# Kernel optimization log

Measured on AMD Instinct MI355X. Metric: run time of the kernel, lower is better.

The kernel has to match this reference:

```python
import jax, jax.numpy as jnp
import numpy as np

NUM_GROUPS = 8
EPS = 1e-5


def group_norm(x, gamma, beta):
    # x: [B, C, H, W]
    B, C, H, W = x.shape
    xg = x.reshape(B, NUM_GROUPS, C // NUM_GROUPS, H, W)
    mean = xg.mean(axis=(2, 3, 4), keepdims=True)
    var = xg.var(axis=(2, 3, 4), keepdims=True)
    xn = (xg - mean) * jax.lax.rsqrt(var + EPS)
    xn = xn.reshape(B, C, H, W)
    return xn * gamma[None, :, None, None] + beta[None, :, None, None]


def setup_inputs() -> dict:
    key = jax.random.key(0)
    ks = jax.random.split(key, 7)
    B, C, H, W = 4, 512, 64, 64
    x = jax.random.normal(ks[0], (B, C, H, W), dtype=jnp.float32)
    gamma = jnp.ones((C,), dtype=jnp.float32)
    beta = jnp.zeros((C,), dtype=jnp.float32)
    w_qkv = jax.random.normal(ks[1], (3 * C, C), dtype=jnp.float32) * (1.0 / np.sqrt(C))
    b_qkv = jax.random.normal(ks[2], (3 * C,), dtype=jnp.float32) * 0.01
    w_proj = jax.random.normal(ks[3], (C, C), dtype=jnp.float32) * (1.0 / np.sqrt(C))
    b_proj = jax.random.normal(ks[4], (C,), dtype=jnp.float32) * 0.01
    return {"x": x, "gamma": gamma, "beta": beta, "w_qkv": w_qkv,
            "b_qkv": b_qkv, "w_proj": w_proj, "b_proj": b_proj}


def reference(x, gamma, beta, w_qkv, b_qkv, w_proj, b_proj):
    B, C, H, W = x.shape
    N = H * W
    h = group_norm(x, gamma, beta)                       # [B,C,H,W]
    hf = h.reshape(B, C, N)                              # [B,C,N]
    # 1x1 conv == channel-wise linear map
    qkv = jnp.einsum('oc,bcn->bon', w_qkv, hf) + b_qkv[None, :, None]  # [B,3C,N]
    q, k, v = jnp.split(qkv, 3, axis=1)                  # each [B,C,N]
    q = q.transpose(0, 2, 1)                             # [B,N,C]
    v = v.transpose(0, 2, 1)                             # [B,N,C]
    scale = C ** (-0.5)
    attn = jax.nn.softmax(jnp.einsum('bnc,bcm->bnm', q, k) * scale, axis=-1)  # [B,N,N]
    out = jnp.einsum('bnm,bmc->bnc', attn, v)            # [B,N,C]
    out = out.transpose(0, 2, 1).reshape(B, C, H, W)
    proj = jnp.einsum('oc,bchw->bohw', w_proj, out) + b_proj[None, :, None, None]
    return x + proj
```

## Files before the change

### kernel.cpp

```cpp
#include <hip/hip_runtime.h>

typedef __attribute__((ext_vector_type(8))) short bf16x8;
typedef __attribute__((ext_vector_type(4))) float f32x4;
typedef __attribute__((ext_vector_type(4))) short s16x4;
using u16 = unsigned short;
using u8 = unsigned char;

#define DEVINL static __device__ __forceinline__

DEVINL u16 f2bf(float f) {
  union { float f; unsigned u; } v; v.f = f;
  unsigned r = v.u + 0x7FFFu + ((v.u >> 16) & 1u);
  return (u16)(r >> 16);
}

DEVINL u8 f2e4m3_sw(float f) {
  union { float f; unsigned u; } v; v.f = f;
  unsigned s = (v.u >> 24) & 0x80u;
  float a = fabsf(f);
  a = fminf(a, 448.f);
  union { float f; unsigned u; } b; b.f = a;
  unsigned bu = b.u + 0x7FFFFu + ((b.u >> 20) & 1u);
  unsigned e = bu >> 23;
  unsigned r;
  if (e >= 121) {
    r = ((e - 120) << 3) | ((bu >> 20) & 7u);
    if (r > 0x7Eu) r = 0x7Eu;
  } else {
    r = (unsigned)(a * 512.f + 0.5f);
    if (r > 7u) r = 8u;
  }
  return (u8)(r | s);
}

#if __has_builtin(__builtin_amdgcn_cvt_pk_fp8_f32)
DEVINL u8 f2e4m3(float f) {
  int p = __builtin_amdgcn_cvt_pk_fp8_f32(f, f, 0, false);
  return (u8)(p & 0xFF);
}
#else
DEVINL u8 f2e4m3(float f) { return f2e4m3_sw(f); }
#endif

DEVINL float bf2f(u16 h) {
  union { unsigned u; float f; } v; v.u = ((unsigned)h) << 16; return v.f;
}

DEVINL void gload16(const u16* g, u16* l) {
  __builtin_amdgcn_global_load_lds((const __attribute__((address_space(1))) void*)g,
                                   (__attribute__((address_space(3))) void*)l,
                                   16, 0, 0);
}
DEVINL void gload16b(const u8* g, u8* l) {
  __builtin_amdgcn_global_load_lds((const __attribute__((address_space(1))) void*)g,
                                   (__attribute__((address_space(3))) void*)l,
                                   16, 0, 0);
}

__global__ __launch_bounds__(256) void gn_stats1_k(const float* __restrict__ x,
                                                   float* __restrict__ psum,
                                                   float* __restrict__ psumsq) {
  const int blk = blockIdx.x;
  const float4* p4 = (const float4*)(x + (size_t)(blk >> 4) * (64 * 4096))
                     + (size_t)(blk & 15) * 4096;
  float s = 0.f, ss = 0.f;
  #pragma unroll
  for (int i = 0; i < 16; ++i) {
    float4 v = p4[i*256 + threadIdx.x];
    s  += v.x + v.y + v.z + v.w;
    ss += v.x*v.x + v.y*v.y + v.z*v.z + v.w*v.w;
  }
  #pragma unroll
  for (int off = 32; off > 0; off >>= 1) {
    s  += __shfl_down(s, off, 64);
    ss += __shfl_down(ss, off, 64);
  }
  __shared__ float rs[4], rss[4];
  const int lane = threadIdx.x & 63, w = threadIdx.x >> 6;
  if (lane == 0) { rs[w] = s; rss[w] = ss; }
  __syncthreads();
  if (threadIdx.x == 0) {
    psum[blk]   = rs[0]+rs[1]+rs[2]+rs[3];
    psumsq[blk] = rss[0]+rss[1]+rss[2]+rss[3];
  }
}

__global__ void gn_stats2_k(const float* __restrict__ psum,
                            const float* __restrict__ psumsq,
                            float* __restrict__ stats) {
  const int bg = threadIdx.x;
  if (bg >= 32) return;
  float s = 0.f, ss = 0.f;
  #pragma unroll
  for (int p = 0; p < 16; ++p) { s += psum[bg*16+p]; ss += psumsq[bg*16+p]; }
  const float inv = 1.f / 262144.f;
  float mean = s * inv;
  float var  = ss * inv - mean * mean;
  stats[bg*2]   = mean;
  stats[bg*2+1] = rsqrtf(var + 1e-5f);
}

__global__ __launch_bounds__(256) void gn_apply_k(const float* __restrict__ x,
                                                  const float* __restrict__ gamma,
                                                  const float* __restrict__ beta,
                                                  const float* __restrict__ stats,
                                                  u16* __restrict__ hT,
                                                  u8* __restrict__ hT8, int useF8) {
  __shared__ u16 tile[64][68];
  const int b = blockIdx.z, ct = blockIdx.y, nt = blockIdx.x;
  const int t = threadIdx.x;
  const float mean = stats[(b*8 + ct)*2 + 0];
  const float rstd = stats[(b*8 + ct)*2 + 1];
  const float* xb = x + ((size_t)b*512 + (size_t)ct*64) * 4096 + nt*64;
  #pragma unroll
  for (int i = 0; i < 4; ++i) {
    int idx = i*256 + t;
    int cl = idx >> 4, nl4 = idx & 15;
    float4 v = *(const float4*)(xb + (size_t)cl*4096 + nl4*4);
    float g = gamma[ct*64 + cl], bb = beta[ct*64 + cl];
    s16x4 o;
    o.x = (short)f2bf((v.x - mean) * rstd * g + bb);
    o.y = (short)f2bf((v.y - mean) * rstd * g + bb);
    o.z = (short)f2bf((v.z - mean) * rstd * g + bb);
    o.w = (short)f2bf((v.w - mean) * rstd * g + bb);
    *(s16x4*)(&tile[cl][nl4*4]) = o;
  }
  __syncthreads();
  if (useF8) {
    u8* o = hT8 + ((size_t)b*4096 + (size_t)nt*64) * 512 + ct*64;
    #pragma unroll
    for (int i = 0; i < 16; ++i) {
      int idx = i*256 + t; int nl = idx >> 6, cl = idx & 63;
      o[(size_t)nl*512 + cl] = f2e4m3(bf2f(tile[cl][nl]));
    }
  } else {
    u16* o = hT + ((size_t)b*4096 + (size_t)nt*64) * 512 + ct*64;
    #pragma unroll
    for (int i = 0; i < 16; ++i) {
      int idx = i*256 + t; int nl = idx >> 6, cl = idx & 63;
      o[(size_t)nl*512 + cl] = tile[cl][nl];
    }
  }
}

__global__ __launch_bounds__(256) void cast_w_k(const float* __restrict__ wq,
                                                const float* __restrict__ wp,
                                                u16* __restrict__ wqb,
                                                u16* __restrict__ wpb,
                                                u8* __restrict__ wq8,
                                                u8* __restrict__ wp8, int useF8) {
  int i = blockIdx.x*256 + threadIdx.x;
  if (useF8) {
    if (i < 1536*512) wq8[i] = f2e4m3(wq[i]);
    if (i < 512*512)  wp8[i] = f2e4m3(wp[i]);
  } else {
    if (i < 1536*512) wqb[i] = f2bf(wq[i]);
    if (i < 512*512)  wpb[i] = f2bf(wp[i]);
  }
}

DEVINL void gemm_nt_core(const u16* __restrict__ A, int lda,
                         const u16* __restrict__ B, int ldb,
                         int K, u16* As, u16* Bs, f32x4 acc[4][4]) {
  const int tid = threadIdx.x;
  const int lane = tid & 63, w = tid >> 6;
  const int wr = w >> 1, wc = w & 1;
  const int fr = lane & 15, fk = lane >> 4;
  for (int kt = 0; kt < K; kt += 64) {
    #pragma unroll
    for (int i = 0; i < 4; ++i) {
      int ch = i*256 + tid;
      int row = ch >> 3, kc = ch & 7;
      gload16(A + (size_t)row*lda + kt + kc*8, As + ch*8);
      gload16(B + (size_t)row*ldb + kt + kc*8, Bs + ch*8);
    }
    __syncthreads();
    #pragma unroll
    for (int kk = 0; kk < 2; ++kk) {
      bf16x8 af[4], bfg[4];
      #pragma unroll
      for (int i = 0; i < 4; ++i)
        af[i] = *(const bf16x8*)(As + ((wr*64 + i*16 + fr)*64 + kk*32 + fk*8));
      #pragma unroll
      for (int j = 0; j < 4; ++j)
        bfg[j] = *(const bf16x8*)(Bs + ((wc*64 + j*16 + fr)*64 + kk*32 + fk*8));
      #pragma unroll
      for (int i = 0; i < 4; ++i)
        #pragma unroll
        for (int j = 0; j < 4; ++j)
          acc[i][j] = __builtin_amdgcn_mfma_f32_16x16x32_bf16(af[i], bfg[j], acc[i][j], 0, 0, 0);
    }
    __syncthreads();
  }
}

#define GEMM_PROLOGUE() \
  __shared__ __align__(16) u16 As[128*64]; \
  __shared__ __align__(16) u16 Bs[128*64]; \
  f32x4 acc[4][4] = {}; \
  const int tid = threadIdx.x; \
  const int lane = tid & 63, w = tid >> 6; \
  const int wr = w >> 1, wc = w & 1; \
  const int fr = lane & 15, fk = lane >> 4; \
  (void)lane;

#define MFMA8(a, b, c) __builtin_amdgcn_mfma_f32_16x16x32_fp8_fp8((a), (b), (c), 0, 0, 0)

DEVINL void gemm_nt_f8(const u8* __restrict__ A, int lda,
                       const u8* __restrict__ B, int ldb,
                       int K, u8* Af, u8* Bf, f32x4 acc[4][4]) {
  const int tid = threadIdx.x;
  const int lane = tid & 63, w = tid >> 6;
  const int wr = w >> 1, wc = w & 1;
  const int fr = lane & 15, fk = lane >> 4;
  for (int kt = 0; kt < K; kt += 128) {
    #pragma unroll
    for (int q = 0; q < 4; ++q) {
      int c = q*256 + tid;
      int row = c >> 3, s16 = c & 7;
      int kc = s16 ^ ((row >> 1) & 7);
      gload16b(A + (size_t)row*lda + kt + kc*16, Af + c*16);
      gload16b(B + (size_t)row*ldb + kt + kc*16, Bf + c*16);
    }
    __syncthreads();
    #pragma unroll
    for (int kk = 0; kk < 4; ++kk) {
      long long a8[4], b8[4];
      #pragma unroll
      for (int i = 0; i < 4; ++i) {
        int row = wr*64 + i*16 + fr;
        int s16r = (kk*2 + (fk>>1)) ^ ((row>>1)&7);
        a8[i] = *(const long long*)(Af + row*128 + (s16r<<4) + ((fk&1)<<3));
      }
      #pragma unroll
      for (int j = 0; j < 4; ++j) {
        int row = wc*64 + j*16 + fr;
        int s16r = (kk*2 + (fk>>1)) ^ ((row>>1)&7);
        b8[j] = *(const long long*)(Bf + row*128 + (s16r<<4) + ((fk&1)<<3));
      }
      #pragma unroll
      for (int i = 0; i < 4; ++i)
        #pragma unroll
        for (int j = 0; j < 4; ++j)
          acc[i][j] = MFMA8(a8[i], b8[j], acc[i][j]);
    }
    __syncthreads();
  }
}

__global__ __launch_bounds__(256) void k_qkv(const u16* __restrict__ hT,
                                             const u16* __restrict__ wq,
                                             const float* __restrict__ bqkv,
                                             u16* __restrict__ qT, u16* __restrict__ kT,
                                             u16* __restrict__ vb) {
  GEMM_PROLOGUE();
  const int bz = blockIdx.z;
  const int rowBase = blockIdx.y * 128, colBase = blockIdx.x * 128;
  gemm_nt_core(hT + ((size_t)bz*4096 + rowBase)*512, 512,
               wq + (size_t)colBase*512, 512, 512, As, Bs, acc);
  #pragma unroll
  for (int i = 0; i < 4; ++i)
    #pragma unroll
    for (int j = 0; j < 4; ++j)
      #pragma unroll
      for (int r = 0; r < 4; ++r) {
        int n = rowBase + wr*64 + i*16 + fk*4 + r;
        int o = colBase + wc*64 + j*16 + fr;
        u16 u = f2bf(acc[i][j][r] + bqkv[o]);
        if (o < 512)       qT[((size_t)bz*4096 + n)*512 + o]          = u;
        else if (o < 1024) kT[((size_t)bz*4096 + n)*512 + (o - 512)]  = u;
        else               vb[((size_t)bz*512 + (o - 1024))*4096 + n] = u;
      }
}

__global__ __launch_bounds__(256) void k_qkv_f8(const u8* __restrict__ hT8,
                                                const u8* __restrict__ wq8,
                                                const float* __restrict__ bqkv,
                                                u8* __restrict__ qF8, u8* __restrict__ kF8,
                                                u8* __restrict__ vF8) {
  __shared__ __align__(16) u8 Af[128*128];
  __shared__ __align__(16) u8 Bf[128*128];
  f32x4 acc[4][4] = {};
  const int tid = threadIdx.x;
  const int lane = tid & 63, w = tid >> 6;
  const int wr = w >> 1, wc = w & 1;
  const int fr = lane & 15, fk = lane >> 4;
  const int bz = blockIdx.z;
  const int rowBase = blockIdx.y * 128, colBase = blockIdx.x * 128;
  gemm_nt_f8(hT8 + ((size_t)bz*4096 + rowBase)*512, 512,
             wq8 + (size_t)colBase*512, 512, 512, Af, Bf, acc);
  #pragma unroll
  for (int i = 0; i < 4; ++i)
    #pragma unroll
    for (int j = 0; j < 4; ++j)
      #pragma unroll
      for (int r = 0; r < 4; ++r) {
        int n = rowBase + wr*64 + i*16 + fk*4 + r;
        int o = colBase + wc*64 + j*16 + fr;
        u8 u = f2e4m3(acc[i][j][r] + bqkv[o]);
        if (o < 512)       qF8[((size_t)bz*4096 + n)*512 + o]          = u;
        else if (o < 1024) kF8[((size_t)bz*4096 + n)*512 + (o - 512)]  = u;
        else               vF8[((size_t)bz*512 + (o - 1024))*4096 + n] = u;
      }
}

__global__ __launch_bounds__(512) void k_scores_f8(const u8* __restrict__ qF8,
                                                   const u8* __restrict__ kF8,
                                                   u8* __restrict__ E8,
                                                   float* __restrict__ lsum) {
  __shared__ __align__(16) u8 Af[128*64];
  __shared__ __align__(16) u8 Bf[128*64];
  f32x4 acc[2][4] = {};
  const int tid = threadIdx.x;
  const int lane = tid & 63, w = tid >> 6;
  const int wr = w >> 1, wc = w & 1;
  const int fr = lane & 15, fk = lane >> 4;
  const int bz = blockIdx.z;
  int f = blockIdx.y * 32 + blockIdx.x;
  int L = (f & 7) * 128 + (f >> 3);
  const int rowBase = (L >> 5) * 128, colBase = (L & 31) * 128;
  const u8* qa = qF8 + (size_t)bz*4096*512 + (size_t)rowBase*512;
  const u8* ka = kF8 + (size_t)bz*4096*512 + (size_t)colBase*512;
  u8* Eb = E8 + (size_t)bz*4096*4096;
  float* ls = lsum + (size_t)bz*4096;

  for (int kt = 0; kt < 512; kt += 64) {
    {
      int c = tid;
      int row = c >> 2, s16 = c & 3;
      int kc = s16 ^ ((row >> 1) & 3);
      gload16b(qa + (size_t)row*512 + kt + kc*16, Af + c*16);
      gload16b(ka + (size_t)row*512 + kt + kc*16, Bf + c*16);
    }
    __syncthreads();
    #pragma unroll
    for (int kk = 0; kk < 2; ++kk) {
      long long a8[2], b8[4];
      #pragma unroll
      for (int i = 0; i < 2; ++i) {
        int row = wr*32 + i*16 + fr;
        a8[i] = *(const long long*)(Af + row*64 +
                ((((kk*2 + (fk>>1)) ^ ((row>>1)&3)) << 4) | ((fk&1) << 3)));
      }
      #pragma unroll
      for (int j = 0; j < 4; ++j) {
        int row = wc*64 + j*16 + fr;
        b8[j] = *(const long long*)(Bf + row*64 +
                ((((kk*2 + (fk>>1)) ^ ((row>>1)&3)) << 4) | ((fk&1) << 3)));
      }
      #pragma unroll
      for (int i = 0; i < 2; ++i)
        #pragma unroll
        for (int j = 0; j < 4; ++j)
          acc[i][j] = MFMA8(a8[i], b8[j], acc[i][j]);
    }
    __syncthreads();
  }

  const float scale = 0.04419417382415922f;
  #pragma unroll
  for (int i = 0; i < 2; ++i)
    #pragma unroll
    for (int r = 0; r < 4; ++r) {
      int nl = rowBase + wr*32 + i*16 + fk*4 + r;
      float s = 0.f;
      #pragma unroll
      for (int j = 0; j < 4; ++j) {
        int m = colBase + wc*64 + j*16 + fr;
        float e = __expf(acc[i][j][r] * scale);
        Eb[(size_t)nl*4096 + m] = f2e4m3(e);
        s += e;
      }
      s += __shfl_xor(s, 1, 64);
      s += __shfl_xor(s, 2, 64);
      s += __shfl_xor(s, 4, 64);
      s += __shfl_xor(s, 8, 64);
      if (fr == 0) atomicAdd(&ls[nl], s);
    }
}

__global__ __launch_bounds__(256) void k_pv_f8(const u8* __restrict__ E8,
                                               const u8* __restrict__ vF8,
                                               const float* __restrict__ lsum,
                                               u8* __restrict__ attn8) {
  __shared__ __align__(16) u8 Af[128*128];
  __shared__ __align__(16) u8 Bf[128*128];
  f32x4 acc[4][4] = {};
  const int tid = threadIdx.x;
  const int lane = tid & 63, w = tid >> 6;
  const int wr = w >> 1, wc = w & 1;
  const int fr = lane & 15, fk = lane >> 4;
  const int bz = blockIdx.z;
  int f = blockIdx.y * 4 + blockIdx.x;
  int L = (f & 7) * 16 + (f >> 3);
  const int rowBase = (L >> 2) * 128, colBase = (L & 3) * 128;
  const u8* Eb = E8 + (size_t)bz*4096*4096 + (size_t)rowBase*4096;
  const u8* vbb = vF8 + (size_t)bz*512*4096 + (size_t)colBase*4096;
  const float* ls = lsum + (size_t)bz*4096;
  u8* ab = attn8 + (size_t)bz*4096*512;

  gemm_nt_f8(Eb, 4096, vbb, 4096, 4096, Af, Bf, acc);

  #pragma unroll
  for (int i = 0; i < 4; ++i)
    #pragma unroll
    for (int r = 0; r < 4; ++r) {
      int nl = rowBase + wr*64 + i*16 + fk*4 + r;
      float rinv = 1.0f / ls[nl];
      #pragma unroll
      for (int j = 0; j < 4; ++j) {
        int d = colBase + wc*64 + j*16 + fr;
        ab[(size_t)nl*512 + d] = f2e4m3(acc[i][j][r] * rinv);
      }
    }
}

__global__ __launch_bounds__(256) void k_proj_f8(const u8* __restrict__ wp8,
                                                 const u8* __restrict__ attn8,
                                                 const float* __restrict__ bproj,
                                                 const float* __restrict__ x,
                                                 float* __restrict__ out) {
  __shared__ __align__(16) u8 Af[128*128];
  __shared__ __align__(16) u8 Bf[128*128];
  f32x4 acc[4][4] = {};
  const int tid = threadIdx.x;
  const int lane = tid & 63, w = tid >> 6;
  const int wr = w >> 1, wc = w & 1;
  const int fr = lane & 15, fk = lane >> 4;
  const int bz = blockIdx.z;
  const int rowBase = blockIdx.y * 128, colBase = blockIdx.x * 128;
  gemm_nt_f8(wp8 + (size_t)rowBase*512, 512,
             attn8 + ((size_t)bz*4096 + colBase)*512, 512, 512, Af, Bf, acc);
  #pragma unroll
  for (int i = 0; i < 4; ++i)
    #pragma unroll
    for (int j = 0; j < 4; ++j)
      #pragma unroll
      for (int r = 0; r < 4; ++r) {
        int o = rowBase + wr*64 + i*16 + fk*4 + r;
        int n = colBase + wc*64 + j*16 + fr;
        size_t idx = ((size_t)bz*512 + o)*4096 + n;
        out[idx] = acc[i][j][r] + bproj[o] + x[idx];
      }
}

__global__ __launch_bounds__(256) void k_scores(const u16* __restrict__ qT,
                                                const u16* __restrict__ kT,
                                                u16* __restrict__ E,
                                                float* __restrict__ lsum,
                                                long long qkStride, long long eStride,
                                                int lsStride) {
  GEMM_PROLOGUE();
  const int bz = blockIdx.z;
  const u16* q0 = qT + (size_t)bz * qkStride;
  const u16* k0 = kT + (size_t)bz * qkStride;
  u16* Eb = E + (size_t)bz * eStride;
  float* ls = lsum + (size_t)bz * lsStride;
  const int rowBase = blockIdx.y * 128, colBase = blockIdx.x * 128;
  gemm_nt_core(q0 + (size_t)rowBase*512, 512, k0 + (size_t)colBase*512, 512,
               512, As, Bs, acc);
  const float scale = 0.04419417382415922f;
  #pragma unroll
  for (int i = 0; i < 4; ++i)
    #pragma unroll
    for (int r = 0; r < 4; ++r) {
      int nl = rowBase + wr*64 + i*16 + fk*4 + r;
      float s = 0.f;
      #pragma unroll
      for (int j = 0; j < 4; ++j) {
        int m = colBase + wc*64 + j*16 + fr;
        float e = __expf(acc[i][j][r] * scale);
        Eb[(size_t)nl*4096 + m] = f2bf(e);
        s += e;
      }
      s += __shfl_xor(s, 1, 64);
      s += __shfl_xor(s, 2, 64);
      s += __shfl_xor(s, 4, 64);
      s += __shfl_xor(s, 8, 64);
      if (fr == 0) atomicAdd(&ls[nl], s);
    }
}

__global__ __launch_bounds__(256) void k_pv(const u16* __restrict__ E,
                                            const u16* __restrict__ vb,
                                            const float* __restrict__ lsum,
                                            u16* __restrict__ attnb,
                                            long long eStride, long long vStride,
                                            int lsStride, long long aStride) {
  GEMM_PROLOGUE();
  const int bz = blockIdx.z;
  const u16* Eb = E + (size_t)bz * eStride;
  const u16* vbb = vb + (size_t)bz * vStride;
  const float* ls = lsum + (size_t)bz * lsStride;
  u16* ab = attnb + (size_t)bz * aStride;
  const int rowBase = blockIdx.y * 128, colBase = blockIdx.x * 128;
  gemm_nt_core(Eb + (size_t)rowBase*4096, 4096, vbb + (size_t)colBase*4096, 4096,
               4096, As, Bs, acc);
  #pragma unroll
  for (int i = 0; i < 4; ++i)
    #pragma unroll
    for (int r = 0; r < 4; ++r) {
      int nl = rowBase + wr*64 + i*16 + fk*4 + r;
      float rinv = 1.0f / ls[nl];
      #pragma unroll
      for (int j = 0; j < 4; ++j) {
        int d = colBase + wc*64 + j*16 + fr;
        ab[(size_t)nl*512 + d] = f2bf(acc[i][j][r] * rinv);
      }
    }
}

__global__ __launch_bounds__(256) void k_proj(const u16* __restrict__ wp,
                                              const u16* __restrict__ attn,
                                              const float* __restrict__ bproj,
                                              const float* __restrict__ x,
                                              float* __restrict__ out) {
  GEMM_PROLOGUE();
  const int bz = blockIdx.z;
  const int rowBase = blockIdx.y * 128, colBase = blockIdx.x * 128;
  gemm_nt_core(wp + (size_t)rowBase*512, 512,
               attn + ((size_t)bz*4096 + colBase)*512, 512, 512, As, Bs, acc);
  #pragma unroll
  for (int i = 0; i < 4; ++i)
    #pragma unroll
    for (int j = 0; j < 4; ++j)
      #pragma unroll
      for (int r = 0; r < 4; ++r) {
        int o = rowBase + wr*64 + i*16 + fk*4 + r;
        int n = colBase + wc*64 + j*16 + fr;
        size_t idx = ((size_t)bz*512 + o)*4096 + n;
        out[idx] = acc[i][j][r] + bproj[o] + x[idx];
      }
}

extern "C" void kernel_launch(void* const* d_in, const int* in_sizes, int n_in,
                              void* d_out, int out_size, void* d_ws, size_t ws_size,
                              hipStream_t stream) {
  const float* x      = (const float*)d_in[0];
  const float* gamma  = (const float*)d_in[1];
  const float* beta   = (const float*)d_in[2];
  const float* w_qkv  = (const float*)d_in[3];
  const float* b_qkv  = (const float*)d_in[4];
  const float* w_proj = (const float*)d_in[5];
  const float* b_proj = (const float*)d_in[6];
  float* out = (float*)d_out;
  char* ws = (char*)d_ws;

  size_t off = 0;
  u16* wqb   = (u16*)(ws + off); off += (size_t)1536*512*2;
  u16* wpb   = (u16*)(ws + off); off += (size_t)512*512*2;
  u8*  wq8   = (u8*)(ws + off);  off += (size_t)1536*512;
  u8*  wp8   = (u8*)(ws + off);  off += (size_t)512*512;
  float* stats = (float*)(ws + off); off += 256;
  float* psum  = (float*)(ws + off); off += 512*4;
  float* psumsq= (float*)(ws + off); off += 512*4;
  float* lsum  = (float*)(ws + off); off += (size_t)4*4096*4;
  u16* hT    = (u16*)(ws + off);
  u16* attn  = hT;
  off += (size_t)4*4096*512*2;
  u16* qT    = (u16*)(ws + off); off += (size_t)4*4096*512*2;
  u16* kT    = (u16*)(ws + off); off += (size_t)4*4096*512*2;
  u16* vb    = (u16*)(ws + off); off += (size_t)4*4096*512*2;
  u16* E     = (u16*)(ws + off);
  size_t avail = ws_size > off ? ws_size - off : 0;
  const int useF8 = (avail >= (size_t)4*4096*4096) ? 1 : 0;
  u8* hT8  = (u8*)hT;
  u8* attn8 = hT8;
  u8* qF8 = (u8*)qT;
  u8* kF8 = (u8*)kT;
  u8* vF8 = (u8*)vb;
  u8* E8  = (u8*)E;

  gn_stats1_k<<<512, 256, 0, stream>>>(x, psum, psumsq);
  gn_stats2_k<<<1, 32, 0, stream>>>(psum, psumsq, stats);
  gn_apply_k<<<dim3(64, 8, 4), 256, 0, stream>>>(x, gamma, beta, stats, hT, hT8, useF8);
  cast_w_k<<<3072, 256, 0, stream>>>(w_qkv, w_proj, wqb, wpb, wq8, wp8, useF8);

  if (useF8) {
    k_qkv_f8<<<dim3(12, 32, 4), 256, 0, stream>>>(hT8, wq8, b_qkv, qF8, kF8, vF8);
    (void)hipMemsetAsync(lsum, 0, (size_t)4*4096*sizeof(float), stream);
    k_scores_f8<<<dim3(32, 32, 4), 512, 0, stream>>>(qF8, kF8, E8, lsum);
    k_pv_f8<<<dim3(4, 32, 4), 256, 0, stream>>>(E8, vF8, lsum, attn8);
    k_proj_f8<<<dim3(32, 4, 4), 256, 0, stream>>>(wp8, attn8, b_proj, x, out);
  } else {
    k_qkv<<<dim3(12, 32, 4), 256, 0, stream>>>(hT, wqb, b_qkv, qT, kT, vb);
    int CH = 4096;
    while (CH > 128 && (size_t)CH*4096*2 > avail) CH >>= 1;
    for (int b = 0; b < 4; ++b) {
      for (int c0 = 0; c0 < 4096; c0 += CH) {
        (void)hipMemsetAsync(lsum, 0, (size_t)CH * sizeof(float), stream);
        k_scores<<<dim3(32, CH/128, 1), 256, 0, stream>>>(
            qT + ((size_t)b*4096 + c0)*512, kT + (size_t)b*4096*512, E, lsum, 0, 0, 0);
        k_pv<<<dim3(4, CH/128, 1), 256, 0, stream>>>(
            E, vb + (size_t)b*512*4096, lsum, attn + ((size_t)b*4096 + c0)*512, 0, 0, 0, 0);
      }
    }
    k_proj<<<dim3(32, 4, 4), 256, 0, stream>>>(wpb, attn, b_proj, x, out);
  }
}
```

Baseline: 249.9 us.

## Compute softmax row sums in PV kernel via MFMA with ones vector

Removes the per-row sum reduction, shuffles and atomics from the scores kernel, along with the lsum memset. The PV kernel now inlines its GEMM loop and adds one extra MFMA per row fragment against an all-ones FP8 operand (0x38 = 1.0 in e4m3), so the row sums come from the quantized E values. This drops the atomic traffic and a launch, at the cost of some extra MFMA work in the PV kernel, with each of the 4 column blocks recomputing the same row sums. It also changes numerics slightly, since the normalization now uses the sum of the FP8-rounded exponentials rather than the FP32 ones.

```diff
diff --git a/kernel.cpp b/kernel.cpp
--- a/kernel.cpp
+++ b/kernel.cpp
@@ -306,8 +306,7 @@
 
 __global__ __launch_bounds__(512) void k_scores_f8(const u8* __restrict__ qF8,
                                                    const u8* __restrict__ kF8,
-                                                   u8* __restrict__ E8,
-                                                   float* __restrict__ lsum) {
+                                                   u8* __restrict__ E8) {
   __shared__ __align__(16) u8 Af[128*64];
   __shared__ __align__(16) u8 Bf[128*64];
   f32x4 acc[2][4] = {};
@@ -322,7 +321,6 @@
   const u8* qa = qF8 + (size_t)bz*4096*512 + (size_t)rowBase*512;
   const u8* ka = kF8 + (size_t)bz*4096*512 + (size_t)colBase*512;
   u8* Eb = E8 + (size_t)bz*4096*4096;
-  float* ls = lsum + (size_t)bz*4096;
 
   for (int kt = 0; kt < 512; kt += 64) {
     {
@@ -363,29 +361,22 @@
     #pragma unroll
     for (int r = 0; r < 4; ++r) {
       int nl = rowBase + wr*32 + i*16 + fk*4 + r;
-      float s = 0.f;
       #pragma unroll
       for (int j = 0; j < 4; ++j) {
         int m = colBase + wc*64 + j*16 + fr;
-        float e = __expf(acc[i][j][r] * scale);
-        Eb[(size_t)nl*4096 + m] = f2e4m3(e);
-        s += e;
-      }
-      s += __shfl_xor(s, 1, 64);
-      s += __shfl_xor(s, 2, 64);
-      s += __shfl_xor(s, 4, 64);
-      s += __shfl_xor(s, 8, 64);
-      if (fr == 0) atomicAdd(&ls[nl], s);
+        Eb[(size_t)nl*4096 + m] = f2e4m3(__expf(acc[i][j][r] * scale));
+      }
     }
 }
 
 __global__ __launch_bounds__(256) void k_pv_f8(const u8* __restrict__ E8,
                                                const u8* __restrict__ vF8,
-                                               const float* __restrict__ lsum,
                                                u8* __restrict__ attn8) {
   __shared__ __align__(16) u8 Af[128*128];
   __shared__ __align__(16) u8 Bf[128*128];
   f32x4 acc[4][4] = {};
+  f32x4 acs[4] = {};
+  const long long ONES = 0x3838383838383838LL;
   const int tid = threadIdx.x;
   const int lane = tid & 63, w = tid >> 6;
   const int wr = w >> 1, wc = w & 1;
@@ -396,17 +387,50 @@
   const int rowBase = (L >> 2) * 128, colBase = (L & 3) * 128;
   const u8* Eb = E8 + (size_t)bz*4096*4096 + (size_t)rowBase*4096;
   const u8* vbb = vF8 + (size_t)bz*512*4096 + (size_t)colBase*4096;
-  const float* ls = lsum + (size_t)bz*4096;
   u8* ab = attn8 + (size_t)bz*4096*512;
 
-  gemm_nt_f8(Eb, 4096, vbb, 4096, 4096, Af, Bf, acc);
+  for (int kt = 0; kt < 4096; kt += 128) {
+    #pragma unroll
+    for (int q = 0; q < 4; ++q) {
+      int c = q*256 + tid;
+      int row = c >> 3, s16 = c & 7;
+      int kc = s16 ^ ((row >> 1) & 7);
+      gload16b(Eb + (size_t)row*4096 + kt + kc*16, Af + c*16);
+      gload16b(vbb + (size_t)row*4096 + kt + kc*16, Bf + c*16);
+    }
+    __syncthreads();
+    #pragma unroll
+    for (int kk = 0; kk < 4; ++kk) {
+      long long a8[4], b8[4];
+      #pragma unroll
+      for (int i = 0; i < 4; ++i) {
+        int row = wr*64 + i*16 + fr;
+        int s16r = (kk*2 + (fk>>1)) ^ ((row>>1)&7);
+        a8[i] = *(const long long*)(Af + row*128 + (s16r<<4) + ((fk&1)<<3));
+      }
+      #pragma unroll
+      for (int j = 0; j < 4; ++j) {
+        int row = wc*64 + j*16 + fr;
+        int s16r = (kk*2 + (fk>>1)) ^ ((row>>1)&7);
+        b8[j] = *(const long long*)(Bf + row*128 + (s16r<<4) + ((fk&1)<<3));
+      }
+      #pragma unroll
+      for (int i = 0; i < 4; ++i) {
+        #pragma unroll
+        for (int j = 0; j < 4; ++j)
+          acc[i][j] = MFMA8(a8[i], b8[j], acc[i][j]);
+        acs[i] = MFMA8(a8[i], ONES, acs[i]);
+      }
+    }
+    __syncthreads();
+  }
 
   #pragma unroll
   for (int i = 0; i < 4; ++i)
     #pragma unroll
     for (int r = 0; r < 4; ++r) {
       int nl = rowBase + wr*64 + i*16 + fk*4 + r;
-      float rinv = 1.0f / ls[nl];
+      float rinv = 1.0f / acs[i][r];
       #pragma unroll
       for (int j = 0; j < 4; ++j) {
         int d = colBase + wc*64 + j*16 + fr;
@@ -578,9 +602,8 @@
 
   if (useF8) {
     k_qkv_f8<<<dim3(12, 32, 4), 256, 0, stream>>>(hT8, wq8, b_qkv, qF8, kF8, vF8);
-    (void)hipMemsetAsync(lsum, 0, (size_t)4*4096*sizeof(float), stream);
-    k_scores_f8<<<dim3(32, 32, 4), 512, 0, stream>>>(qF8, kF8, E8, lsum);
-    k_pv_f8<<<dim3(4, 32, 4), 256, 0, stream>>>(E8, vF8, lsum, attn8);
+    k_scores_f8<<<dim3(32, 32, 4), 512, 0, stream>>>(qF8, kF8, E8);
+    k_pv_f8<<<dim3(4, 32, 4), 256, 0, stream>>>(E8, vF8, attn8);
     k_proj_f8<<<dim3(32, 4, 4), 256, 0, stream>>>(wp8, attn8, b_proj, x, out);
   } else {
     k_qkv<<<dim3(12, 32, 4), 256, 0, stream>>>(hT, wqb, b_qkv, qT, kT, vb);
```

New measurement: 219.9 us. 12.0% less time.
